# Kernel optimization log

Hardware: AMD Instinct MI355X
Metric: run time of the kernel (lower is better)

## Reference

```python
import jax, jax.numpy as jnp
import numpy as np

DIM = 2048
H = 16
HD = 128
S = 2640          # frame_seq_len(22*40=880) * num_frame_per_block(3)
CACHE = 5280      # 6 cached frames
MAXPOS = 8192
EPS = 1e-6


def rmsnorm(x, g, eps=EPS):
    return x * jax.lax.rsqrt(jnp.mean(x * x, axis=-1, keepdims=True) + eps) * g


def apply_rope_interleaved(x, cos, sin):
    # x: [s, H, HD]; cos/sin: [s, HD//2]; is_neox=False -> adjacent pairs
    x1 = x[..., 0::2]
    x2 = x[..., 1::2]
    c = cos[:, None, :]
    s_ = sin[:, None, :]
    o1 = x1 * c - x2 * s_
    o2 = x2 * c + x1 * s_
    return jnp.stack([o1, o2], axis=-1).reshape(x.shape)


def setup_inputs() -> dict:
    key = jax.random.key(0)
    ks = jax.random.split(key, 10)
    w_scale = DIM ** -0.5
    x = jax.random.normal(ks[0], (1, S, DIM), dtype=jnp.float32)
    # cos_sin_cache: [max_pos, HD] = [cos(HD//2) | sin(HD//2)], real rope values
    inv_freq = 1.0 / (10000.0 ** (np.arange(0, HD, 2, dtype=np.float32) / HD))
    t = np.arange(MAXPOS, dtype=np.float32)
    ang = np.outer(t, inv_freq)  # [MAXPOS, HD//2]
    freqs = jnp.asarray(np.concatenate([np.cos(ang), np.sin(ang)], axis=1), dtype=jnp.float32)
    k_cache = jax.random.normal(ks[1], (CACHE, H, HD), dtype=jnp.float32)
    v_cache = jax.random.normal(ks[2], (CACHE, H, HD), dtype=jnp.float32)
    Wq = jax.random.normal(ks[3], (DIM, DIM), dtype=jnp.float32) * w_scale
    Wk = jax.random.normal(ks[4], (DIM, DIM), dtype=jnp.float32) * w_scale
    Wv = jax.random.normal(ks[5], (DIM, DIM), dtype=jnp.float32) * w_scale
    Wo = jax.random.normal(ks[6], (DIM, DIM), dtype=jnp.float32) * w_scale
    bq = jnp.zeros((DIM,), jnp.float32)
    bk = jnp.zeros((DIM,), jnp.float32)
    bv = jnp.zeros((DIM,), jnp.float32)
    bo = jnp.zeros((DIM,), jnp.float32)
    gq = jnp.ones((DIM,), jnp.float32)
    gk = jnp.ones((DIM,), jnp.float32)
    return {"x": x, "freqs": freqs, "k_cache": k_cache, "v_cache": v_cache,
            "Wq": Wq, "bq": bq, "Wk": Wk, "bk": bk, "Wv": Wv, "bv": bv,
            "Wo": Wo, "bo": bo, "gq": gq, "gk": gk, "current_start": CACHE}


def reference(x, freqs, k_cache, v_cache, Wq, bq, Wk, bk, Wv, bv, Wo, bo, gq, gk, current_start):
    s = x.shape[1]
    xf = x[0]                                   # [s, DIM], B==1
    q = rmsnorm(xf @ Wq.T + bq, gq).reshape(s, H, HD)
    k = rmsnorm(xf @ Wk.T + bk, gk).reshape(s, H, HD)
    v = (xf @ Wv.T + bv).reshape(s, H, HD)
    # fused RoPE via cos_sin_cache lookup, interleaved (is_neox=False)
    positions = jnp.arange(s, dtype=jnp.int32) + current_start
    cs = freqs[positions]                       # [s, HD]
    cos, sin = cs[:, : HD // 2], cs[:, HD // 2:]
    rq = apply_rope_interleaved(q, cos, sin)
    rk = apply_rope_interleaved(k, cos, sin)
    # streaming attention: full access to cache, causal within incoming block
    k_all = jnp.concatenate([k_cache, rk], axis=0)  # [L, H, HD]
    v_all = jnp.concatenate([v_cache, v], axis=0)
    L = k_all.shape[0]
    scale = HD ** -0.5
    scores = jnp.einsum("qhd,khd->hqk", rq, k_all) * scale  # [H, s, L]
    kv_idx = jnp.arange(L)
    q_idx = jnp.arange(s)
    mask = (kv_idx[None, :] - (L - s)) <= q_idx[:, None]    # cache always visible
    scores = jnp.where(mask[None, :, :], scores, jnp.float32(-1e30))
    attn = jax.nn.softmax(scores, axis=-1)
    out = jnp.einsum("hqk,khd->qhd", attn, v_all).reshape(s, DIM)
    y = out @ Wo.T + bo
    return y[None]                              # [1, s, DIM]
```

## Files before the change

kernel.cpp:

```cpp
#include <hip/hip_runtime.h>

#define DIMN 2048
#define NH 16
#define HDIM 128

typedef __attribute__((ext_vector_type(4))) float f32x4;
typedef __attribute__((ext_vector_type(16))) float f32x16;
typedef __attribute__((ext_vector_type(8))) __bf16 bfx8;
typedef __attribute__((ext_vector_type(4))) __bf16 bf16x4;
typedef __attribute__((ext_vector_type(8))) unsigned short u16x8;

__device__ __forceinline__ unsigned short f2bf(float f){
  unsigned u = __builtin_bit_cast(unsigned, f);
  u += 0x7fffu + ((u >> 16) & 1u);
  return (unsigned short)(u >> 16);
}
__device__ __forceinline__ float bf2f(unsigned short h){
  unsigned u = (unsigned)h << 16;
  return __builtin_bit_cast(float, u);
}

__device__ __forceinline__ void gl_lds16(const void* g, void* l){
  __builtin_amdgcn_global_load_lds((const __attribute__((address_space(1))) void*)g,
                                   (__attribute__((address_space(3))) void*)l, 16, 0, 0);
}

__device__ __forceinline__ int xcd_swz(int bid, int nwg){
  const int q = nwg >> 3, r = nwg & 7;
  const int xcd = bid & 7, idx = bid >> 3;
  return (xcd < r ? xcd*(q+1) : r*(q+1) + (xcd-r)*q) + idx;
}

#define MFMA16(a,b,c) __builtin_amdgcn_mfma_f32_16x16x32_bf16((a),(b),(c),0,0,0)
#define MFMA32(a,b,c) __builtin_amdgcn_mfma_f32_32x32x16_bf16((a),(b),(c),0,0,0)

__global__ __launch_bounds__(256) void prep_kernel(const float* __restrict__ x,
    const float* __restrict__ Wq, const float* __restrict__ Wk, const float* __restrict__ Wv,
    const float* __restrict__ Wo, const float* __restrict__ k_cache,
    const float* __restrict__ v_cache,
    unsigned short* __restrict__ xb, unsigned short* __restrict__ Wqb,
    unsigned short* __restrict__ Wkb, unsigned short* __restrict__ Wvb,
    unsigned short* __restrict__ Wob, unsigned short* __restrict__ kb,
    unsigned short* __restrict__ vtb, int S_, int CACHE_, int L_){
  __shared__ __align__(16) unsigned short tile[32][72];
  const int WB = (DIMN*DIMN/8)/256;
  const int t = threadIdx.x;
  int bid = blockIdx.x;
  if (bid < S_){
    const size_t base = (size_t)bid*DIMN + t*8;
    const float4* p = (const float4*)(x + base);
    float4 a = p[0], b = p[1];
    u16x8 o;
    o[0]=f2bf(a.x); o[1]=f2bf(a.y); o[2]=f2bf(a.z); o[3]=f2bf(a.w);
    o[4]=f2bf(b.x); o[5]=f2bf(b.y); o[6]=f2bf(b.z); o[7]=f2bf(b.w);
    *(u16x8*)(xb + base) = o;
    return;
  }
  bid -= S_;
  if (bid < 4*WB){
    const int wsel = bid / WB;
    const int lb   = bid - wsel*WB;
    const float* in = (wsel==0) ? Wq : (wsel==1) ? Wk : (wsel==2) ? Wv : Wo;
    unsigned short* out = (wsel==0) ? Wqb : (wsel==1) ? Wkb : (wsel==2) ? Wvb : Wob;
    const size_t base = ((size_t)lb*256 + t)*8;
    const float4* p = (const float4*)(in + base);
    float4 a = p[0], b = p[1];
    u16x8 o;
    o[0]=f2bf(a.x); o[1]=f2bf(a.y); o[2]=f2bf(a.z); o[3]=f2bf(a.w);
    o[4]=f2bf(b.x); o[5]=f2bf(b.y); o[6]=f2bf(b.z); o[7]=f2bf(b.w);
    *(u16x8*)(out + base) = o;
    return;
  }
  bid -= 4*WB;
  if (bid < CACHE_){
    const size_t idx = ((size_t)bid*256 + t)*8;
    const int k   = (int)(idx >> 11);
    const int rem = (int)(idx & 2047);
    const int hh  = rem >> 7, d = rem & 127;
    const float4* p = (const float4*)(k_cache + idx);
    float4 a = p[0], b = p[1];
    u16x8 o;
    o[0]=f2bf(a.x); o[1]=f2bf(a.y); o[2]=f2bf(a.z); o[3]=f2bf(a.w);
    o[4]=f2bf(b.x); o[5]=f2bf(b.y); o[6]=f2bf(b.z); o[7]=f2bf(b.w);
    *(u16x8*)(kb + (size_t)hh*L_*HDIM + (size_t)k*HDIM + d) = o;
    return;
  }
  bid -= CACHE_;
  {
    const int nkb = (CACHE_ + 63) >> 6;
    const int kbi = bid % nkb;
    const int rest = bid / nkb;
    const int dbi = rest & 3;
    const int hh  = rest >> 2;
    const int kb0 = kbi * 64, db0 = dbi * 32;
    const int kk = t >> 2, dd = (t & 3) * 8;
    const int k = kb0 + kk;
    if (k < CACHE_){
      const float* p = v_cache + (size_t)k*DIMN + hh*HDIM + db0 + dd;
      float4 a = ((const float4*)p)[0], b = ((const float4*)p)[1];
      tile[dd+0][kk] = f2bf(a.x); tile[dd+1][kk] = f2bf(a.y);
      tile[dd+2][kk] = f2bf(a.z); tile[dd+3][kk] = f2bf(a.w);
      tile[dd+4][kk] = f2bf(b.x); tile[dd+5][kk] = f2bf(b.y);
      tile[dd+6][kk] = f2bf(b.z); tile[dd+7][kk] = f2bf(b.w);
    }
    __syncthreads();
    const int d = t >> 3, k0 = (t & 7) * 8;
    unsigned short* dst = vtb + (size_t)hh*HDIM*L_ + (size_t)(db0+d)*L_ + kb0 + k0;
    if (kb0 + k0 + 8 <= CACHE_){
      *(u16x8*)dst = *(const u16x8*)&tile[d][k0];
    } else {
      #pragma unroll
      for (int e=0;e<8;++e) if (kb0 + k0 + e < CACHE_) dst[e] = tile[d][k0+e];
    }
  }
}

__global__ __launch_bounds__(256) void vtrans_bf16_kernel(const unsigned short* __restrict__ src,
    unsigned short* __restrict__ vt, int R, int koff, int L_){
  __shared__ __align__(16) unsigned short tile[32][72];
  const int kb0 = blockIdx.x * 64, db0 = blockIdx.y * 32, hh = blockIdx.z;
  const int t = threadIdx.x;
  const int kk = t >> 2, dd = (t & 3) * 8;
  const int k = kb0 + kk;
  if (k < R){
    u16x8 a = *(const u16x8*)(src + (size_t)k*DIMN + hh*HDIM + db0 + dd);
    #pragma unroll
    for (int e=0;e<8;++e) tile[dd+e][kk] = a[e];
  }
  __syncthreads();
  const int d = t >> 3, k0 = (t & 7) * 8;
  unsigned short* dst = vt + (size_t)hh*HDIM*L_ + (size_t)(db0+d)*L_ + koff + kb0 + k0;
  if (kb0 + k0 + 8 <= R){
    *(u16x8*)dst = *(const u16x8*)&tile[d][k0];
  } else {
    #pragma unroll
    for (int e=0;e<8;++e) if (kb0 + k0 + e < R) dst[e] = tile[d][k0+e];
  }
}

__global__ __launch_bounds__(256) void norm_rope_kernel(const unsigned short* __restrict__ lin0,
    const unsigned short* __restrict__ lin1, const float* __restrict__ gq,
    const float* __restrict__ gk, const float* __restrict__ freqs, const int* __restrict__ cur,
    unsigned short* __restrict__ qb, unsigned short* __restrict__ kb,
    int S_, int CACHE_, int L_, float qsc){
  const int q = blockIdx.x, t = threadIdx.x;
  const int path = blockIdx.y;
  const unsigned short* lin = path ? lin1 : lin0;
  const float* g = path ? gk : gq;
  unsigned short* out = path ? kb : qb;
  const size_t head_stride = path ? (size_t)L_*HDIM : (size_t)S_*HDIM;
  const int row_off = path ? CACHE_ : 0;
  const float oscale = path ? 1.0f : qsc;
  u16x8 v = *(const u16x8*)(lin + (size_t)q*DIMN + t*8);
  float x[8];
  #pragma unroll
  for (int e=0;e<8;++e) x[e] = bf2f(v[e]);
  float ss = 0.f;
  #pragma unroll
  for (int e=0;e<8;++e) ss += x[e]*x[e];
  for (int m=1;m<64;m<<=1) ss += __shfl_xor(ss, m);
  __shared__ float red[4];
  if ((t & 63) == 0) red[t>>6] = ss;
  __syncthreads();
  const float tot = red[0]+red[1]+red[2]+red[3];
  const float rstd = rsqrtf(tot * (1.0f/2048.0f) + 1e-6f);
  const int n0 = t*8;
  float xr[8];
  #pragma unroll
  for (int e=0;e<8;++e) xr[e] = x[e] * rstd * g[n0+e];
  const int pos = cur[0] + q;
  const int hh = n0 >> 7, d0 = n0 & 127;
  const float* fr = freqs + (size_t)pos * HDIM;
  float o[8];
  #pragma unroll
  for (int p=0;p<4;++p){
    const int j = (d0>>1) + p;
    const float c = fr[j], s = fr[64+j];
    o[2*p]   = xr[2*p]*c - xr[2*p+1]*s;
    o[2*p+1] = xr[2*p+1]*c + xr[2*p]*s;
  }
  u16x8 ov;
  #pragma unroll
  for (int e=0;e<8;++e) ov[e] = f2bf(o[e]*oscale);
  *(u16x8*)(out + (size_t)hh*head_stride + (size_t)(q+row_off)*HDIM + d0) = ov;
}

__global__ __launch_bounds__(256,2) void gemm_bt(const unsigned short* __restrict__ A,
    const unsigned short* __restrict__ B, const float* __restrict__ bias,
    float* __restrict__ C, int M, int N, int K){
  __shared__ __align__(16) unsigned short As[2][128*64];
  __shared__ __align__(16) unsigned short Bs[2][128*64];
  const int mb = (M + 127) >> 7;
  const int swz = xcd_swz(blockIdx.x, gridDim.x);
  const int bx = swz / mb, by = swz % mb;
  const int t = threadIdx.x;
  const int w = t >> 6, lane = t & 63, lh = lane >> 4, ll = lane & 15;
  const int wr = w >> 1, wc = w & 1;
  const int m0 = by * 128, n0 = bx * 128;
  const int srow = t >> 3;
  const int scb  = (t & 7) * 16;
  const int swc  = (scb ^ ((srow & 7) << 4)) >> 1;
  int arow[4]; size_t brow[4];
  #pragma unroll
  for (int c=0;c<4;++c){
    int r = m0 + c*32 + srow; if (r >= M) r = M-1;
    arow[c] = r;
    brow[c] = (size_t)(n0 + c*32 + srow);
  }
  const int xsw = (ll & 7) << 4;
  f32x4 acc[4][4] = {};
  const int nk = K >> 6;
  auto stage = [&](int b, int kt){
    const int k0 = kt << 6;
    #pragma unroll
    for (int c=0;c<4;++c){
      gl_lds16(A + (size_t)arow[c]*K + k0 + swc, (char*)As[b] + c*4096 + w*1024);
      gl_lds16(B + brow[c]*K       + k0 + swc, (char*)Bs[b] + c*4096 + w*1024);
    }
  };
  stage(0, 0);
  asm volatile("s_waitcnt vmcnt(0)" ::: "memory");
  __syncthreads();
  int cur = 0;
  for (int kt = 0; kt < nk; ++kt){
    if (kt + 1 < nk) stage(cur ^ 1, kt + 1);
    #pragma unroll
    for (int kk=0;kk<2;++kk){
      const int cb = kk*64 + lh*16;
      bfx8 a[4], b[4];
      #pragma unroll
      for (int i=0;i<4;++i)
        a[i] = *(const bfx8*)((const char*)As[cur] + (wr*64 + i*16 + ll)*128 + (cb ^ xsw));
      #pragma unroll
      for (int j=0;j<4;++j)
        b[j] = *(const bfx8*)((const char*)Bs[cur] + (wc*64 + j*16 + ll)*128 + (cb ^ xsw));
      __builtin_amdgcn_s_setprio(1);
      #pragma unroll
      for (int i=0;i<4;++i)
        #pragma unroll
        for (int j=0;j<4;++j)
          acc[i][j] = MFMA16(a[i], b[j], acc[i][j]);
      __builtin_amdgcn_s_setprio(0);
    }
    asm volatile("s_waitcnt vmcnt(0)" ::: "memory");
    __syncthreads();
    cur ^= 1;
  }
  #pragma unroll
  for (int i=0;i<4;++i){
    #pragma unroll
    for (int j=0;j<4;++j){
      const int col = n0 + wc*64 + j*16 + ll;
      const float bb = bias[col];
      #pragma unroll
      for (int r=0;r<4;++r){
        const int row = m0 + wr*64 + i*16 + lh*4 + r;
        if (row < M) C[(size_t)row*N + col] = acc[i][j][r] + bb;
      }
    }
  }
}

__global__ __launch_bounds__(256,2) void gemm_qkv(const unsigned short* __restrict__ A,
    const unsigned short* __restrict__ B0, const unsigned short* __restrict__ B1,
    const unsigned short* __restrict__ B2, const float* __restrict__ g0,
    const float* __restrict__ g1, const float* __restrict__ g2,
    unsigned short* __restrict__ C0, unsigned short* __restrict__ C1,
    unsigned short* __restrict__ C2, int M, int N, int K){
  const int mb = (M + 127) >> 7;
  const int nxt = N >> 7;
  const int per = nxt * mb;
  const int swz = xcd_swz(blockIdx.x, gridDim.x);
  const int zz = swz / per;
  const int rem = swz - zz * per;
  const int bx = rem / mb, by = rem % mb;
  const unsigned short* B = (zz==0) ? B0 : (zz==1) ? B1 : B2;
  const float* bias       = (zz==0) ? g0 : (zz==1) ? g1 : g2;
  unsigned short* C       = (zz==0) ? C0 : (zz==1) ? C1 : C2;
  __shared__ __align__(16) unsigned short As[2][128*64];
  __shared__ __align__(16) unsigned short Bs[2][128*64];
  const int t = threadIdx.x;
  const int w = t >> 6, lane = t & 63, lh = lane >> 4, ll = lane & 15;
  const int wr = w >> 1, wc = w & 1;
  const int m0 = by * 128, n0 = bx * 128;
  const int srow = t >> 3;
  const int scb  = (t & 7) * 16;
  const int swc  = (scb ^ ((srow & 7) << 4)) >> 1;
  int arow[4]; size_t brow[4];
  #pragma unroll
  for (int c=0;c<4;++c){
    int r = m0 + c*32 + srow; if (r >= M) r = M-1;
    arow[c] = r;
    brow[c] = (size_t)(n0 + c*32 + srow);
  }
  const int xsw = (ll & 7) << 4;
  f32x4 acc[4][4] = {};
  const int nk = K >> 6;
  auto stage = [&](int b, int kt){
    const int k0 = kt << 6;
    #pragma unroll
    for (int c=0;c<4;++c){
      gl_lds16(A + (size_t)arow[c]*K + k0 + swc, (char*)As[b] + c*4096 + w*1024);
      gl_lds16(B + brow[c]*K       + k0 + swc, (char*)Bs[b] + c*4096 + w*1024);
    }
  };
  stage(0, 0);
  asm volatile("s_waitcnt vmcnt(0)" ::: "memory");
  __syncthreads();
  int cur = 0;
  for (int kt = 0; kt < nk; ++kt){
    if (kt + 1 < nk) stage(cur ^ 1, kt + 1);
    #pragma unroll
    for (int kk=0;kk<2;++kk){
      const int cb = kk*64 + lh*16;
      bfx8 a[4], b[4];
      #pragma unroll
      for (int i=0;i<4;++i)
        a[i] = *(const bfx8*)((const char*)As[cur] + (wr*64 + i*16 + ll)*128 + (cb ^ xsw));
      #pragma unroll
      for (int j=0;j<4;++j)
        b[j] = *(const bfx8*)((const char*)Bs[cur] + (wc*64 + j*16 + ll)*128 + (cb ^ xsw));
      __builtin_amdgcn_s_setprio(1);
      #pragma unroll
      for (int i=0;i<4;++i)
        #pragma unroll
        for (int j=0;j<4;++j)
          acc[i][j] = MFMA16(a[i], b[j], acc[i][j]);
      __builtin_amdgcn_s_setprio(0);
    }
    asm volatile("s_waitcnt vmcnt(0)" ::: "memory");
    __syncthreads();
    cur ^= 1;
  }
  #pragma unroll
  for (int i=0;i<4;++i){
    #pragma unroll
    for (int j=0;j<4;++j){
      const int col = n0 + wc*64 + j*16 + ll;
      const float bb = bias[col];
      #pragma unroll
      for (int r=0;r<4;++r){
        const int row = m0 + wr*64 + i*16 + lh*4 + r;
        if (row < M) C[(size_t)row*N + col] = f2bf(acc[i][j][r] + bb);
      }
    }
  }
}

__global__ __launch_bounds__(256,2) void attn_kernel(const unsigned short* __restrict__ Q,
    const unsigned short* __restrict__ K, const unsigned short* __restrict__ VT,
    unsigned short* __restrict__ O, float* __restrict__ pacc, float* __restrict__ pml,
    int S_, int L_, int CLn, int nx, int nsplit){
  __shared__ __align__(16) unsigned short Ks[2][64*128];
  __shared__ __align__(16) unsigned short Vs[2][128*64];
  __shared__ __align__(16) unsigned short Ps[4][32*64];
  const int nwg = gridDim.x;
  const int swzid = (blockIdx.x & 7)*(nwg >> 3) + (blockIdx.x >> 3);
  const int xq = swzid % nx;
  const int rest = swzid / nx;
  const int hh = rest % NH;
  const int z  = rest / NH;
  const int q0 = xq * 128;
  const int t = threadIdx.x, w = t >> 6, lane = t & 63;
  const int l31 = lane & 31, h = lane >> 5;
  char* Pw = (char*)Ps[w];
  const int xswp = (l31 & 7) << 4;
  const unsigned short* Qh = Q  + (size_t)hh*S_*HDIM;
  const unsigned short* Kh = K  + (size_t)hh*L_*HDIM;
  const unsigned short* Vh = VT + (size_t)hh*HDIM*L_;
  const int wrow0 = q0 + w*32;
  const int myq = wrow0 + l31;
  bfx8 qf[8];
  {
    int qr = myq; if (qr >= S_) qr = S_ - 1;
    #pragma unroll
    for (int kk=0;kk<8;++kk)
      qf[kk] = *(const bfx8*)(Qh + (size_t)qr*HDIM + kk*16 + h*8);
  }
  f32x16 acc[4] = {};
  float m_st = -1e20f, l_st = 0.f;
  int qlast = q0 + 127; if (qlast >= S_) qlast = S_ - 1;
  const int kend = CLn + qlast + 1;
  const int nt = (kend + 63) >> 6;
  const int tps = (nt + nsplit - 1) / nsplit;
  const int t0 = z * tps;
  int t1 = t0 + tps; if (t1 > nt) t1 = nt;
  const int ksrow = t >> 4;
  const int kswc  = (((t & 15)*16) ^ ((ksrow & 7) << 4)) >> 1;
  const int vsrow = t >> 3;
  const int vswc  = (((t & 7)*16) ^ ((vsrow & 7) << 4)) >> 1;

  auto stage = [&](int b, int ktile){
    const int kv0 = ktile << 6;
    #pragma unroll
    for (int c=0;c<4;++c)
      gl_lds16(Kh + (size_t)(kv0 + c*16 + ksrow)*HDIM + kswc, (char*)Ks[b] + c*4096 + w*1024);
    #pragma unroll
    for (int c=0;c<4;++c)
      gl_lds16(Vh + (size_t)(c*32 + vsrow)*L_ + kv0 + vswc, (char*)Vs[b] + c*4096 + w*1024);
  };

  if (t0 < t1) stage(0, t0);
  asm volatile("s_waitcnt vmcnt(0)" ::: "memory");
  __syncthreads();
  const int krow0 = l31,      koff0 = (krow0 & 7) << 4;
  const int krow1 = 32 + l31, koff1 = (krow1 & 7) << 4;
  int cur = 0;
  for (int kt = t0; kt < t1; ++kt){
    const int kv0 = kt << 6;
    if (kt + 1 < t1) stage(cur ^ 1, kt + 1);
    const char* Kc = (const char*)Ks[cur];
    const char* Vc = (const char*)Vs[cur];
    f32x16 sc0 = {}, sc1 = {};
    __builtin_amdgcn_s_setprio(1);
    #pragma unroll
    for (int kk=0;kk<8;++kk){
      const int cb = kk*32 + h*16;
      bfx8 kf0 = *(const bfx8*)(Kc + krow0*256 + (cb ^ koff0));
      bfx8 kf1 = *(const bfx8*)(Kc + krow1*256 + (cb ^ koff1));
      sc0 = MFMA32(kf0, qf[kk], sc0);
      sc1 = MFMA32(kf1, qf[kk], sc1);
    }
    __builtin_amdgcn_s_setprio(0);
    if (kv0 + 63 > CLn + wrow0){
      const int lim = CLn + myq;
      #pragma unroll
      for (int r=0;r<16;++r){
        const int kl = (r&3) + 8*(r>>2) + 4*h;
        if (kv0 + kl      > lim) sc0[r] = -1e30f;
        if (kv0 + 32 + kl > lim) sc1[r] = -1e30f;
      }
    }
    float mt = sc0[0];
    #pragma unroll
    for (int r=1;r<15;r+=2) mt = fmaxf(fmaxf(sc0[r], sc0[r+1]), mt);
    mt = fmaxf(sc0[15], mt);
    #pragma unroll
    for (int r=0;r<16;r+=2) mt = fmaxf(fmaxf(sc1[r], sc1[r+1]), mt);
    mt = fmaxf(mt, __shfl_xor(mt, 32));
    mt = fmaxf(mt, -1e20f);
    if (!__all(mt - m_st <= 11.54f)){
      const float mn = fmaxf(m_st, mt);
      const float corr = exp2f(m_st - mn);
      m_st = mn;
      l_st *= corr;
      #pragma unroll
      for (int r=0;r<16;++r){
        const int qrow = (r&3) + 8*(r>>2) + 4*h;
        const float ca = __shfl(corr, qrow);
        #pragma unroll
        for (int db=0;db<4;++db) acc[db][r] *= ca;
      }
    }
    float rs = 0.f;
    #pragma unroll
    for (int r=0;r<16;++r){
      const float p0 = exp2f(sc0[r] - m_st);
      const float p1 = exp2f(sc1[r] - m_st);
      sc0[r] = p0; sc1[r] = p1;
      rs += p0 + p1;
    }
    rs += __shfl_xor(rs, 32);
    l_st += rs;
    #pragma unroll
    for (int i=0;i<4;++i){
      bf16x4 p0 = { (__bf16)sc0[4*i], (__bf16)sc0[4*i+1], (__bf16)sc0[4*i+2], (__bf16)sc0[4*i+3] };
      bf16x4 p1 = { (__bf16)sc1[4*i], (__bf16)sc1[4*i+1], (__bf16)sc1[4*i+2], (__bf16)sc1[4*i+3] };
      const int kb0b = (8*i + 4*h) * 2;
      *(bf16x4*)(Pw + l31*128 + (kb0b        ^ xswp)) = p0;
      *(bf16x4*)(Pw + l31*128 + ((64 + kb0b) ^ xswp)) = p1;
    }
    __builtin_amdgcn_s_setprio(1);
    #pragma unroll
    for (int s=0;s<4;++s){
      bfx8 pa = *(const bfx8*)(Pw + l31*128 + ((s*32 + h*16) ^ xswp));
      const int vb = s*32 + h*16;
      #pragma unroll
      for (int db=0;db<4;++db){
        const int vrow = db*32 + l31;
        bfx8 vf = *(const bfx8*)(Vc + vrow*128 + (vb ^ ((vrow & 7) << 4)));
        acc[db] = MFMA32(pa, vf, acc[db]);
      }
    }
    __builtin_amdgcn_s_setprio(0);
    asm volatile("s_waitcnt vmcnt(0)" ::: "memory");
    __syncthreads();
    cur ^= 1;
  }
  if (nsplit == 1){
    const float linv = 1.0f / l_st;
    #pragma unroll
    for (int r=0;r<16;++r){
      const int qrow = (r&3) + 8*(r>>2) + 4*h;
      const float inv = __shfl(linv, qrow);
      const int qr = wrow0 + qrow;
      if (qr < S_){
        #pragma unroll
        for (int db=0;db<4;++db)
          O[(size_t)qr*DIMN + hh*HDIM + db*32 + l31] = f2bf(acc[db][r]*inv);
      }
    }
  } else {
    #pragma unroll
    for (int r=0;r<16;++r){
      const int qrow = (r&3) + 8*(r>>2) + 4*h;
      const int qr = wrow0 + qrow;
      if (qr < S_){
        const size_t rid = ((size_t)z*NH + hh)*S_ + qr;
        float* dst = pacc + rid*128;
        #pragma unroll
        for (int db=0;db<4;++db) dst[db*32 + l31] = acc[db][r];
      }
    }
    if (lane < 32 && myq < S_){
      const size_t rid2 = ((size_t)z*NH + hh)*S_ + myq;
      pml[rid2*2]   = m_st;
      pml[rid2*2+1] = l_st;
    }
  }
}

__global__ __launch_bounds__(256) void combine_kernel(const float* __restrict__ pacc,
    const float* __restrict__ pml, unsigned short* __restrict__ ob, int S_, int nsplit){
  const int t = threadIdx.x;
  const int rid = blockIdx.x*2 + (t >> 7);
  if (rid >= S_*NH) return;
  const int d = t & 127;
  const int hh = rid / S_;
  const int q  = rid - hh*S_;
  float M = -1e20f;
  for (int s=0; s<nsplit; ++s)
    M = fmaxf(M, pml[((size_t)s*NH*S_ + rid)*2]);
  float lt = 0.f, o = 0.f;
  for (int s=0; s<nsplit; ++s){
    const float m = pml[((size_t)s*NH*S_ + rid)*2];
    const float l = pml[((size_t)s*NH*S_ + rid)*2 + 1];
    const float wgt = exp2f(m - M);
    lt += l * wgt;
    o  += pacc[((size_t)s*NH*S_ + rid)*128 + d] * wgt;
  }
  if (lt == 0.f) lt = 1.f;
  ob[(size_t)q*DIMN + hh*HDIM + d] = f2bf(o / lt);
}

extern "C" void kernel_launch(void* const* d_in, const int* in_sizes, int n_in,
                              void* d_out, int out_size, void* d_ws, size_t ws_size,
                              hipStream_t stream){
  const float* x       = (const float*)d_in[0];
  const float* freqs   = (const float*)d_in[1];
  const float* k_cache = (const float*)d_in[2];
  const float* v_cache = (const float*)d_in[3];
  const float* Wq = (const float*)d_in[4];
  const float* bq = (const float*)d_in[5];
  const float* Wk = (const float*)d_in[6];
  const float* bk = (const float*)d_in[7];
  const float* Wv = (const float*)d_in[8];
  const float* bv = (const float*)d_in[9];
  const float* Wo = (const float*)d_in[10];
  const float* bo = (const float*)d_in[11];
  const float* gq = (const float*)d_in[12];
  const float* gk = (const float*)d_in[13];
  const int*   cur = (const int*)d_in[14];

  const int S = in_sizes[0] / DIMN;
  const int CACHE_ = in_sizes[2] / DIMN;
  const int L = CACHE_ + S;
  const int CLn = L - S;

  auto al = [](size_t n){ return (n + 255) & ~(size_t)255; };
  char* base = (char*)d_ws;
  size_t off = 0;
  auto take = [&](size_t n){ char* r = base + off; off += al(n); return r; };
  unsigned short* xb  = (unsigned short*)take((size_t)S*DIMN*2);
  unsigned short* Wob = (unsigned short*)take((size_t)DIMN*DIMN*2);
  unsigned short* qb  = (unsigned short*)take((size_t)NH*S*HDIM*2);
  unsigned short* kb  = (unsigned short*)take((size_t)NH*L*HDIM*2);
  unsigned short* vtb = (unsigned short*)take((size_t)NH*HDIM*L*2);
  unsigned short* ob  = (unsigned short*)take((size_t)S*DIMN*2);
  const size_t ubase = off;
  const size_t l_sz = al((size_t)S*DIMN*2);
  const size_t w_sz = al((size_t)DIMN*DIMN*2);
  unsigned short* lin0 = (unsigned short*)(base + ubase);
  unsigned short* lin1 = (unsigned short*)(base + ubase + l_sz);
  unsigned short* lin2 = (unsigned short*)(base + ubase + 2*l_sz);
  unsigned short* Wqb  = (unsigned short*)(base + ubase + 3*l_sz);
  unsigned short* Wkb  = (unsigned short*)(base + ubase + 3*l_sz + w_sz);
  unsigned short* Wvb  = (unsigned short*)(base + ubase + 3*l_sz + 2*w_sz);
  const size_t trans_sz = 3*l_sz + 3*w_sz;
  auto pool_sz = [&](int ns){
    return al((size_t)ns*NH*S*HDIM*4) + al((size_t)ns*NH*S*2*4);
  };
  int nsplit = 1;
  if (ubase + (trans_sz > pool_sz(4) ? trans_sz : pool_sz(4)) <= ws_size) nsplit = 4;
  else if (ubase + (trans_sz > pool_sz(2) ? trans_sz : pool_sz(2)) <= ws_size) nsplit = 2;
  if (ubase + trans_sz > ws_size) return;
  float* pacc = (float*)(base + ubase);
  float* pml  = (float*)(base + ubase + al((size_t)nsplit*NH*S*HDIM*4));

  const int WB = (DIMN*DIMN/8)/256;
  const int nkb = (CACHE_ + 63) >> 6;
  const int prep_blocks = S + 4*WB + CACHE_ + nkb*4*NH;
  prep_kernel<<<prep_blocks, 256, 0, stream>>>(x, Wq, Wk, Wv, Wo, k_cache, v_cache,
                                               xb, Wqb, Wkb, Wvb, Wob, kb, vtb,
                                               S, CACHE_, L);

  const int mb = (S+127)/128;
  gemm_qkv<<<(DIMN/128)*mb*3, 256, 0, stream>>>(xb, Wqb, Wkb, Wvb, bq, bk, bv,
                                                lin0, lin1, lin2, S, DIMN, DIMN);
  const float qsc = 0.08838834764831845f * 1.4426950408889634f;
  norm_rope_kernel<<<dim3(S,2), 256, 0, stream>>>(lin0, lin1, gq, gk, freqs, cur,
                                                  qb, kb, S, CACHE_, L, qsc);
  vtrans_bf16_kernel<<<dim3((S+63)/64, 4, NH), 256, 0, stream>>>(lin2, vtb, S, CACHE_, L);

  const int nx = (S+127)/128;
  attn_kernel<<<nx*NH*nsplit, 256, 0, stream>>>(qb, kb, vtb, ob,
                                                pacc, pml, S, L, CLn, nx, nsplit);
  if (nsplit > 1)
    combine_kernel<<<(S*NH+1)/2, 256, 0, stream>>>(pacc, pml, ob, S, nsplit);
  gemm_bt<<<(DIMN/128)*mb, 256, 0, stream>>>(ob, Wob, bo, (float*)d_out, S, DIMN, DIMN);
}
```

Baseline: 470.3 us.

## Single-buffer K/V in attention with split staging to raise occupancy

Replaces the double-buffered K and V shared-memory tiles with single buffers. K for the next tile is loaded after the QK^T MFMAs and V after the PV MFMAs, each behind its own barrier. This shrinks LDS use so the launch bound can rise from 2 to 3 workgroups per CU, trading some in-workgroup load/compute overlap for more concurrent waves. The extra barriers per iteration and the narrower overlap window may expose more memory latency.

```diff
diff --git a/kernel.cpp b/kernel.cpp
--- a/kernel.cpp
+++ b/kernel.cpp
@@ -347,12 +347,12 @@
   }
 }
 
-__global__ __launch_bounds__(256,2) void attn_kernel(const unsigned short* __restrict__ Q,
+__global__ __launch_bounds__(256,3) void attn_kernel(const unsigned short* __restrict__ Q,
     const unsigned short* __restrict__ K, const unsigned short* __restrict__ VT,
     unsigned short* __restrict__ O, float* __restrict__ pacc, float* __restrict__ pml,
     int S_, int L_, int CLn, int nx, int nsplit){
-  __shared__ __align__(16) unsigned short Ks[2][64*128];
-  __shared__ __align__(16) unsigned short Vs[2][128*64];
+  __shared__ __align__(16) unsigned short Ks[64*128];
+  __shared__ __align__(16) unsigned short Vs[128*64];
   __shared__ __align__(16) unsigned short Ps[4][32*64];
   const int nwg = gridDim.x;
   const int swzid = (blockIdx.x & 7)*(nwg >> 3) + (blockIdx.x >> 3);
@@ -390,38 +390,43 @@
   const int vsrow = t >> 3;
   const int vswc  = (((t & 7)*16) ^ ((vsrow & 7) << 4)) >> 1;
 
-  auto stage = [&](int b, int ktile){
+  auto stage_K = [&](int ktile){
     const int kv0 = ktile << 6;
     #pragma unroll
     for (int c=0;c<4;++c)
-      gl_lds16(Kh + (size_t)(kv0 + c*16 + ksrow)*HDIM + kswc, (char*)Ks[b] + c*4096 + w*1024);
+      gl_lds16(Kh + (size_t)(kv0 + c*16 + ksrow)*HDIM + kswc, (char*)Ks + c*4096 + w*1024);
+  };
+  auto stage_V = [&](int ktile){
+    const int kv0 = ktile << 6;
     #pragma unroll
     for (int c=0;c<4;++c)
-      gl_lds16(Vh + (size_t)(c*32 + vsrow)*L_ + kv0 + vswc, (char*)Vs[b] + c*4096 + w*1024);
+      gl_lds16(Vh + (size_t)(c*32 + vsrow)*L_ + kv0 + vswc, (char*)Vs + c*4096 + w*1024);
   };
 
-  if (t0 < t1) stage(0, t0);
-  asm volatile("s_waitcnt vmcnt(0)" ::: "memory");
-  __syncthreads();
+  if (t0 < t1){ stage_K(t0); stage_V(t0); }
+  asm volatile("s_waitcnt vmcnt(4)" ::: "memory");
+  __builtin_amdgcn_sched_barrier(0);
+  __builtin_amdgcn_s_barrier();
+
   const int krow0 = l31,      koff0 = (krow0 & 7) << 4;
   const int krow1 = 32 + l31, koff1 = (krow1 & 7) << 4;
-  int cur = 0;
   for (int kt = t0; kt < t1; ++kt){
     const int kv0 = kt << 6;
-    if (kt + 1 < t1) stage(cur ^ 1, kt + 1);
-    const char* Kc = (const char*)Ks[cur];
-    const char* Vc = (const char*)Vs[cur];
     f32x16 sc0 = {}, sc1 = {};
     __builtin_amdgcn_s_setprio(1);
     #pragma unroll
     for (int kk=0;kk<8;++kk){
       const int cb = kk*32 + h*16;
-      bfx8 kf0 = *(const bfx8*)(Kc + krow0*256 + (cb ^ koff0));
-      bfx8 kf1 = *(const bfx8*)(Kc + krow1*256 + (cb ^ koff1));
+      bfx8 kf0 = *(const bfx8*)((const char*)Ks + krow0*256 + (cb ^ koff0));
+      bfx8 kf1 = *(const bfx8*)((const char*)Ks + krow1*256 + (cb ^ koff1));
       sc0 = MFMA32(kf0, qf[kk], sc0);
       sc1 = MFMA32(kf1, qf[kk], sc1);
     }
     __builtin_amdgcn_s_setprio(0);
+    asm volatile("s_waitcnt vmcnt(0) lgkmcnt(0)" ::: "memory");
+    __builtin_amdgcn_sched_barrier(0);
+    __builtin_amdgcn_s_barrier();
+    if (kt + 1 < t1) stage_K(kt + 1);
     if (kv0 + 63 > CLn + wrow0){
       const int lim = CLn + myq;
       #pragma unroll
@@ -478,14 +483,15 @@
       #pragma unroll
       for (int db=0;db<4;++db){
         const int vrow = db*32 + l31;
-        bfx8 vf = *(const bfx8*)(Vc + vrow*128 + (vb ^ ((vrow & 7) << 4)));
+        bfx8 vf = *(const bfx8*)((const char*)Vs + vrow*128 + (vb ^ ((vrow & 7) << 4)));
         acc[db] = MFMA32(pa, vf, acc[db]);
       }
     }
     __builtin_amdgcn_s_setprio(0);
-    asm volatile("s_waitcnt vmcnt(0)" ::: "memory");
-    __syncthreads();
-    cur ^= 1;
+    asm volatile("s_waitcnt vmcnt(0) lgkmcnt(0)" ::: "memory");
+    __builtin_amdgcn_sched_barrier(0);
+    __builtin_amdgcn_s_barrier();
+    if (kt + 1 < t1) stage_V(kt + 1);
   }
   if (nsplit == 1){
     const float linv = 1.0f / l_st;
```

After: 504.8 us. +7.3%, slower.
